# Optimization experiments

Hardware: AMD Instinct MI355X
Metric: run time of the kernel (lower is better)

## Reference

```python
import jax, jax.numpy as jnp
import numpy as np

B0, K, H, W = 8, 1, 512, 512
S, CS, NMS, M = 25, 51, 5, 2048
REG_W, COV_POW = 1.0, 0.5

def _gauss_kernel(n):
    x = jnp.linspace(-1.0, 1.0, n)
    g = jnp.exp(-x * x / 0.5)
    return g / g.sum()

def _conv1d2d(x, k1d, horizontal, pad_h, pad_w):
    # x: [B,1,H,W]; replicates torch F.conv2d with the given (possibly asymmetric) padding
    kern = k1d.reshape(1, 1, 1, -1) if horizontal else k1d.reshape(1, 1, -1, 1)
    return jax.lax.conv_general_dilated(x, kern, (1, 1), [(pad_h, pad_h), (pad_w, pad_w)],
                                        dimension_numbers=("NCHW", "OIHW", "NCHW"))

def bilinear_sample(img, pts):
    # img [B,C,H,W], pts [B,N,2] (x,y in [-1,1]); grid_sample bilinear, align_corners=False, zero padding
    Bb, C, Hh, Ww = img.shape
    x = (pts[..., 0] + 1.0) * 0.5 * Ww - 0.5
    y = (pts[..., 1] + 1.0) * 0.5 * Hh - 0.5
    x0 = jnp.floor(x); y0 = jnp.floor(y)
    wx = x - x0; wy = y - y0
    x0i = x0.astype(jnp.int32); y0i = y0.astype(jnp.int32)
    flat = img.reshape(Bb, C, Hh * Ww)
    def tap(yi, xi, w):
        ok = ((yi >= 0) & (yi < Hh) & (xi >= 0) & (xi < Ww)).astype(img.dtype)
        idx = jnp.clip(yi, 0, Hh - 1) * Ww + jnp.clip(xi, 0, Ww - 1)  # [B,N]
        v = jnp.take_along_axis(flat, idx[:, None, :], axis=2)        # [B,C,N]
        return v * (w * ok)[:, None, :]
    return (tap(y0i, x0i, (1 - wy) * (1 - wx)) + tap(y0i, x0i + 1, (1 - wy) * wx)
            + tap(y0i + 1, x0i, wy * (1 - wx)) + tap(y0i + 1, x0i + 1, wy * wx))

def compute_matchability(keypoint_p, has_depth, Bt):
    G = _gauss_kernel(S)
    # NOTE: faithful to original asymmetric padding bug: pad H while convolving along W, then pad W while convolving along H
    s = _conv1d2d(keypoint_p.reshape(Bt, 1, H, W), G, True, S // 2, 0)
    s = _conv1d2d(s, G, False, 0, S // 2)
    log_p_hat = jax.nn.log_softmax(jnp.log(s.reshape(Bt, H * W) + 1e-8), axis=-1)
    sd = _conv1d2d(has_depth.reshape(Bt, 1, H, W), G, True, 0, S // 2)
    sd = _conv1d2d(sd, G, False, S // 2, 0).reshape(Bt, H * W)
    p = sd / sd.sum(-1, keepdims=True)
    return jnp.sum(jnp.where(p > 0, p * (jnp.log(jnp.maximum(p, 1e-30)) - log_p_hat), 0.0), axis=-1)

def sample_keypoints(sm):
    # sm [B,H,W]; coverage-reweighted NMS + top-k (topk=True, subpixel=False)
    wcov = jnp.exp(-jnp.square(jnp.linspace(-2.0, 2.0, CS)))
    ld = _conv1d2d(((sm + 1e-6) * 1e4)[:, None], wcov, True, 0, CS // 2)
    ld = _conv1d2d(ld, wcov, False, CS // 2, 0)[:, 0]
    sm = sm * (ld + 1e-8) ** (-COV_POW)
    p = NMS // 2
    mx = jax.lax.reduce_window(sm, -jnp.inf, jax.lax.max, (1, NMS, NMS), (1, 1, 1),
                               [(0, 0), (p, p), (p, p)])
    sm = sm * (sm == mx)
    _, inds = jax.lax.top_k(sm.reshape(-1, H * W), M)
    xs = (jnp.arange(W) + 0.5) * 2.0 / W - 1.0
    ys = (jnp.arange(H) + 0.5) * 2.0 / H - 1.0
    grid = jnp.stack(jnp.meshgrid(xs, ys, indexing="xy"), axis=-1).reshape(H * W, 2)
    return jnp.take(grid, inds, axis=0)  # [B,M,2] normalized (x,y)

def masked_log_softmax(logits, mask):
    return jax.nn.log_softmax(jnp.where(mask, logits, -1e9), axis=-1)

def _reward(d):
    return jnp.exp(-100.0 * d)

def _forward(scoremap, gt_warp_A2B, gt_warp_B2A, valid_A2B, valid_B2A, has_depth):
    sg = jax.lax.stop_gradient
    lA = scoremap[:B0].reshape(B0, K, H * W)
    lB = scoremap[B0:].reshape(B0, K, H * W)
    logits = jnp.concatenate([lA, lB], 0)                                   # [2B,K,HW]
    kp_p = jax.nn.softmax(logits.reshape(2 * B0, K * H * W), -1).reshape(2 * B0, K, H * W).sum(1)
    match_loss = compute_matchability(kp_p, sg(has_depth), 2 * B0).mean()
    # sparse branch is under torch.set_grad_enabled(False)
    kpts_A = sample_keypoints(sg(kp_p[:B0]).reshape(B0, H, W))
    kpts_B = sample_keypoints(sg(kp_p[B0:]).reshape(B0, H, W))
    kpts_A2B = bilinear_sample(sg(gt_warp_A2B[..., 2:]).transpose(0, 3, 1, 2), kpts_A).transpose(0, 2, 1)
    kpts_B2A = bilinear_sample(sg(gt_warp_B2A[..., 2:]).transpose(0, 3, 1, 2), kpts_B).transpose(0, 2, 1)
    legit_A2B = bilinear_sample(sg(valid_A2B)[:, None], kpts_A)[:, 0] > 0   # [B,M]
    legit_B2A = bilinear_sample(sg(valid_B2A)[:, None], kpts_B)[:, 0] > 0
    dA = jnp.sqrt(jnp.sum(jnp.square(kpts_A2B[:, :, None] - kpts_B[:, None]), -1) + 1e-12).min(-1)
    dB = jnp.sqrt(jnp.sum(jnp.square(kpts_B2A[:, :, None] - kpts_A[:, None]), -1) + 1e-12).min(-1)
    rA = _reward(dA); rB = _reward(dB)
    slA = bilinear_sample(lA.reshape(B0, 1, H, W), kpts_A)[:, 0]            # [B,M]
    slB = bilinear_sample(lB.reshape(B0, 1, H, W), kpts_B)[:, 0]
    lpA = masked_log_softmax(slA, legit_A2B)
    lpB = masked_log_softmax(slB, legit_B2A)
    sparse = -jnp.sum(jnp.where(legit_A2B, rA * lpA, 0.0)) - jnp.sum(jnp.where(legit_B2A, rB * lpB, 0.0))
    return sparse + REG_W * match_loss

def setup_inputs() -> dict:
    key = jax.random.key(0)
    ks = jax.random.split(key, 6)
    scoremap = jax.random.normal(ks[0], (2 * B0, K, H, W), jnp.float32)
    gt_warp_A2B = jax.random.uniform(ks[1], (B0, H, W, 4), jnp.float32, -1.0, 1.0)
    gt_warp_B2A = jax.random.uniform(ks[2], (B0, H, W, 4), jnp.float32, -1.0, 1.0)
    valid_A2B = (jax.random.uniform(ks[3], (B0, H, W)) > 0.3).astype(jnp.float32)
    valid_B2A = (jax.random.uniform(ks[4], (B0, H, W)) > 0.3).astype(jnp.float32)
    has_depth = (jax.random.uniform(ks[5], (2 * B0, H, W)) > 0.3).astype(jnp.float32)
    return dict(scoremap=scoremap, gt_warp_A2B=gt_warp_A2B, gt_warp_B2A=gt_warp_B2A,
                valid_A2B=valid_A2B, valid_B2A=valid_B2A, has_depth=has_depth)

def reference(scoremap, gt_warp_A2B, gt_warp_B2A, valid_A2B, valid_B2A, has_depth):
    return _forward(scoremap, gt_warp_A2B, gt_warp_B2A, valid_A2B, valid_B2A, has_depth)
```

## Files before the change

### kernel.cpp

```cpp
#include <hip/hip_runtime.h>

#define HH 512
#define WW 512
#define HW_ 262144
#define NIMG 16
#define MK 2048
#define CAPB 4096
#define SCAP 32768
#define SBUFN 768

static constexpr size_t OFF_B1    = 16777216;
static constexpr size_t OFF_SMALL = 50331648;
static constexpr size_t OFF_SEL  = 4194304;
static constexpr size_t OFF_BND  = 4325376;
static constexpr size_t OFF_PP   = 4849664;
static constexpr size_t OFF_WXp  = 5111808;
static constexpr size_t OFF_WYp  = 5242880;
static constexpr size_t OFF_LG   = 5373952;
static constexpr size_t OFF_SL   = 5505024;
static constexpr size_t OFF_PMIN = 5636096;
static constexpr size_t OFF_HIST = 33554432;
static constexpr size_t OFF_SURV = 33554432 + 4194304;

#define CSTRIDE 32

__device__ __forceinline__ float wred64(float v) {
  for (int m = 1; m < 64; m <<= 1) v += __shfl_xor(v, m);
  return v;
}

__device__ __forceinline__ void g25_wave0(float* g) {
  int t = threadIdx.x;
  if (t < 64) {
    float raw = 0.0f;
    if (t < 25) {
      float x = -1.0f + (float)t * (2.0f / 24.0f);
      raw = expf(-(x * x) / 0.5f);
    }
    float s = raw;
    for (int m = 1; m < 64; m <<= 1) s += __shfl_xor(s, m);
    if (t < 25) g[t] = raw / s;
  }
}
__device__ __forceinline__ void w51_wave0(float* wc) {
  int t = threadIdx.x;
  if (t < 51) {
    float x = -2.0f + (float)t * (4.0f / 50.0f);
    wc[t] = expf(-x * x);
  }
}

template<int B>
__device__ __forceinline__ float brsum(float v, float* red) {
  int t = threadIdx.x;
  red[t] = v; __syncthreads();
  for (int s = B >> 1; s > 0; s >>= 1) {
    if (t < s) red[t] += red[t + s];
    __syncthreads();
  }
  float r = red[0]; __syncthreads();
  return r;
}
template<int B>
__device__ __forceinline__ float brmax(float v, float* red) {
  int t = threadIdx.x;
  red[t] = v; __syncthreads();
  for (int s = B >> 1; s > 0; s >>= 1) {
    if (t < s) red[t] = fmaxf(red[t], red[t + s]);
    __syncthreads();
  }
  float r = red[0]; __syncthreads();
  return r;
}

__global__ void __launch_bounds__(256)
k_pre(const float* __restrict__ x, const float* __restrict__ hd, float* A,
      float* sume, float* sumS, float* Zb) {
  __shared__ float g[25];
  __shared__ float gp[26];
  __shared__ float red[12];
  int tid = threadIdx.x;
  g25_wave0(g);
  if (tid == 0) {
    float c = 0.0f;
    gp[0] = 0.0f;
    for (int k = 0; k < 25; k++) { c += g[k]; gp[k + 1] = c; }
  }
  size_t base = (size_t)blockIdx.x * 1024;
  size_t e = base + tid * 4;
  float4 xs = *(const float4*)(x + e);
  float4 hs = *(const float4*)(hd + e);
  __syncthreads();
  int rem = (int)(e & (HW_ - 1));
  int y = rem >> 9, x0 = rem & 511;
  float wv;
  {
    int k0 = y - 499; if (k0 < 0) k0 = 0;
    int k1 = y + 12;  if (k1 > 24) k1 = 24;
    wv = gp[k1 + 1] - gp[k0];
  }
  float cwv[4], cpv[4];
#pragma unroll
  for (int q = 0; q < 4; q++) {
    int i = x0 + q;
    int lo = i - 487; if (lo < 0) lo = 0;
    int hi = i;       if (hi > 24) hi = 24;
    cwv[q] = gp[hi + 1] - gp[lo];
    int lo2 = i - 499; if (lo2 < 0) lo2 = 0;
    int hi2 = i + 12;  if (hi2 > 24) hi2 = 24;
    cpv[q] = gp[hi2 + 1] - gp[lo2];
  }
  float e0 = expf(xs.x), e1 = expf(xs.y), e2 = expf(xs.z), e3 = expf(xs.w);
  *(float4*)(A + e) = make_float4(e0, e1, e2, e3);
  float r0 = (e0 + e1) + (e2 + e3);
  float r1 = (e0 * cwv[0] + e1 * cwv[1] + e2 * cwv[2] + e3 * cwv[3]) * wv;
  float r2 = (hs.x * cpv[0] + hs.y * cpv[1] + hs.z * cpv[2] + hs.w * cpv[3]) * wv;
  r0 = wred64(r0); r1 = wred64(r1); r2 = wred64(r2);
  int wid = tid >> 6;
  if ((tid & 63) == 0) { red[wid] = r0; red[4 + wid] = r1; red[8 + wid] = r2; }
  __syncthreads();
  if (tid == 0) {
    int img = (int)(base >> 18);
    atomicAdd(&sume[img * CSTRIDE], red[0] + red[1] + red[2] + red[3]);
    atomicAdd(&sumS[img * CSTRIDE], red[4] + red[5] + red[6] + red[7]);
    atomicAdd(&Zb[img * CSTRIDE], red[8] + red[9] + red[10] + red[11]);
  }
}

__global__ void __launch_bounds__(256)
k_hconv(const float* __restrict__ A, const float* __restrict__ hd,
        const float* __restrict__ sume, float* b12) {
  __shared__ __align__(16) float ta[512];
  __shared__ __align__(16) float th[536];
  __shared__ float g[25];
  int tid = threadIdx.x;
  int blk = blockIdx.x;
  int img = blk >> 9;
  size_t rowoff = (size_t)blk * 512;
  g25_wave0(g);
  ((float2*)ta)[tid] = *(const float2*)(A + rowoff + tid * 2);
  ((float2*)(th + 12))[tid] = *(const float2*)(hd + rowoff + tid * 2);
  if (tid < 12) { th[tid] = 0.0f; th[524 + tid] = 0.0f; }
  __syncthreads();
  float inv = 1.0f / sume[img * CSTRIDE];
  int j = 2 * tid;
  float v1a = 0.0f, v1b = 0.0f;
  if (tid >= 6 && tid <= 249) {
    float w[26];
#pragma unroll
    for (int d = 0; d < 26; d++) w[d] = ta[j - 12 + d];
#pragma unroll
    for (int d = 0; d < 25; d++) {
      v1a = fmaf(g[d], w[d], v1a);
      v1b = fmaf(g[d], w[d + 1], v1b);
    }
  }
  float v2a = 0.0f, v2b = 0.0f;
  {
    float u[26];
#pragma unroll
    for (int d = 0; d < 26; d++) u[d] = th[j + d];
#pragma unroll
    for (int d = 0; d < 25; d++) {
      v2a = fmaf(g[d], u[d], v2a);
      v2b = fmaf(g[d], u[d + 1], v2b);
    }
  }
  *(float4*)(b12 + (rowoff + j) * 2) =
      make_float4(v1a * inv, v2a, v1b * inv, v2b);
}

__global__ void __launch_bounds__(256)
k_match(const float* __restrict__ b12,
        const float* __restrict__ sume, const float* sumS, const float* Zb,
        float* macc) {
  __shared__ float g[40];
  __shared__ float red4[4];
  int tid = threadIdx.x;
  g25_wave0(g);
  if (tid >= 25 && tid < 40) g[tid] = 0.0f;
  int blk = blockIdx.x;
  int img = blk >> 6;
  int ty = (blk >> 3) & 7;
  int tx = blk & 7;
  int y0 = ty * 64, x0 = tx * 64;
  const float* base12 = b12 + (size_t)img * HW_ * 2;
  float Z = Zb[img * CSTRIDE];
  float invs = 1.0f / sume[img * CSTRIDE];
  float logS = logf(sumS[img * CSTRIDE] * invs + (float)HW_ * 1e-8f);
  __syncthreads();
  int seg = tid >> 6;
  int c = tid & 63;
  int r0 = seg * 16;
  const float* colp = base12 + (size_t)(x0 + c) * 2;
  float s[16], d[16], wreg[16];
#pragma unroll
  for (int jj = 0; jj < 16; jj++) { s[jj] = 0.f; d[jj] = 0.f; wreg[jj] = 0.f; }
  int ybase = y0 + r0 - 12;
#pragma unroll
  for (int i = 0; i < 40; i++) {
    int y = ybase + i;
    float vx = 0.0f, vy = 0.0f;
    if ((unsigned)y < 512u) {
      float2 v = *(const float2*)(colp + (size_t)y * 1024);
      vx = v.x; vy = v.y;
    }
#pragma unroll
    for (int jj = 15; jj >= 1; jj--) wreg[jj] = wreg[jj - 1];
    wreg[0] = g[i];
#pragma unroll
    for (int jj = 0; jj < 16; jj++) {
      s[jj] = fmaf(wreg[jj], vx, s[jj]);
      d[jj] = fmaf(wreg[jj], vy, d[jj]);
    }
  }
  float acc = 0.0f;
#pragma unroll
  for (int jj = 0; jj < 16; jj++) {
    float p = d[jj] / Z;
    if (p > 0.0f)
      acc += p * (logf(fmaxf(p, 1e-30f)) - (logf(s[jj] + 1e-8f) - logS));
  }
  acc = wred64(acc);
  if ((tid & 63) == 0) red4[tid >> 6] = acc;
  __syncthreads();
  if (tid == 0)
    atomicAdd(macc, red4[0] + red4[1] + red4[2] + red4[3]);
}

__global__ void __launch_bounds__(256)
k_h51(const float* __restrict__ A, const float* __restrict__ sume, float* out,
      unsigned* __restrict__ hist) {
  __shared__ float wc[51];
  __shared__ __align__(16) float ta[564];
  int tid = threadIdx.x;
  int blk = blockIdx.x;
  int img = blk >> 9;
  size_t rowoff = (size_t)blk * 512;
  w51_wave0(wc);
  if (tid < 32)
    ((uint4*)hist)[(size_t)blk * 32 + tid] = make_uint4(0u, 0u, 0u, 0u);
  float s1 = 1e4f / sume[img * CSTRIDE];
  for (int i = tid; i < 562; i += 256) {
    int j = i - 25;
    ta[i] = ((unsigned)j < 512u) ? fmaf(A[rowoff + j], s1, 1e-2f) : 0.0f;
  }
  __syncthreads();
  int j = 2 * tid;
  float w[52];
#pragma unroll
  for (int d = 0; d < 52; d++) w[d] = ta[j + d];
  float va = 0.0f, vb = 0.0f;
#pragma unroll
  for (int d = 0; d < 51; d++) {
    va = fmaf(wc[d], w[d], va);
    vb = fmaf(wc[d], w[d + 1], vb);
  }
  ((float2*)out)[blk * 256 + tid] = make_float2(va, vb);
}

__global__ void __launch_bounds__(512, 6)
k_smwnms(const float* __restrict__ A, const float* __restrict__ sume,
         const float* __restrict__ b1,
         unsigned long long* surv, unsigned* scnt, unsigned* hist) {
  __shared__ float wc[53];
  __shared__ __align__(16) float tb1[119 * 68];
  __shared__ __align__(16) float tsm[68 * 68];
  __shared__ unsigned lcnt;
  __shared__ unsigned gbase;
  float* hm = tb1;
  unsigned long long* sbuf = (unsigned long long*)(tb1 + 4352);
  int tid = threadIdx.x;
  w51_wave0(wc);
  if (tid == 51 || tid == 52) wc[tid] = 0.0f;
  if (tid == 0) lcnt = 0;
  int blk = blockIdx.x;
  int img = blk >> 6;
  int ty = (blk >> 3) & 7;
  int tx = blk & 7;
  int y0 = ty * 64, x0 = tx * 64;
  const float* base = b1 + (size_t)img * HW_;
  {
    float2 vreg[8];
    int laddr[8];
#pragma unroll
    for (int k = 0; k < 8; k++) {
      int i = tid + k * 512;
      bool ok = (i < 119 * 34);
      int r = i / 34, c2 = i - r * 34;
      int y = y0 + r - 27;
      int x = x0 + c2 * 2 - 2;
      float2 v = make_float2(0.0f, 0.0f);
      if (ok && (unsigned)y < 512u && (unsigned)x < 512u)
        v = *(const float2*)(base + (size_t)y * 512 + x);
      vreg[k] = v;
      laddr[k] = ok ? (r * 68 + c2 * 2) : -1;
    }
#pragma unroll
    for (int k = 0; k < 8; k++)
      if (laddr[k] >= 0) *(float2*)(tb1 + laddr[k]) = vreg[k];
  }
  __syncthreads();
  float inv = 1.0f / sume[img * CSTRIDE];
  const float* abase = A + (size_t)img * HW_;
  if (tid < 23 * 17) {
    int rg = tid / 17, cg = tid - rg * 17;
    int r0 = rg * 3, c0 = cg * 4;
    int nr = (r0 <= 65) ? 3 : 2;
    float2 apre[3][2];
#pragma unroll
    for (int jj = 0; jj < 3; jj++) {
      int y = y0 + r0 + jj - 2;
      int xb = x0 + c0 - 2;
      apre[jj][0] = make_float2(0.f, 0.f);
      apre[jj][1] = make_float2(0.f, 0.f);
      if ((unsigned)y < 512u) {
        const float* ar = abase + (size_t)y * 512;
        if ((unsigned)xb < 512u) apre[jj][0] = *(const float2*)(ar + xb);
        if ((unsigned)(xb + 2) < 512u) apre[jj][1] = *(const float2*)(ar + xb + 2);
      }
    }
    float a0x = 0.f, a0y = 0.f, a0z = 0.f, a0w = 0.f;
    float a1x = 0.f, a1y = 0.f, a1z = 0.f, a1w = 0.f;
    float a2x = 0.f, a2y = 0.f, a2z = 0.f, a2w = 0.f;
    float w1 = 0.f, w2 = 0.f;
    const float* tp = tb1 + r0 * 68 + c0;
#pragma unroll 4
    for (int i = 0; i < 53; i++) {
      float4 v = *(const float4*)(tp + i * 68);
      float w0 = wc[i];
      a0x = fmaf(w0, v.x, a0x); a0y = fmaf(w0, v.y, a0y);
      a0z = fmaf(w0, v.z, a0z); a0w = fmaf(w0, v.w, a0w);
      a1x = fmaf(w1, v.x, a1x); a1y = fmaf(w1, v.y, a1y);
      a1z = fmaf(w1, v.z, a1z); a1w = fmaf(w1, v.w, a1w);
      a2x = fmaf(w2, v.x, a2x); a2y = fmaf(w2, v.y, a2y);
      a2z = fmaf(w2, v.z, a2z); a2w = fmaf(w2, v.w, a2w);
      w2 = w1; w1 = w0;
    }
    auto storerow = [&](int jj, float ax, float ay, float az, float aw,
                        float2 p0, float2 p1) {
      int r = r0 + jj;
      int y = y0 + r - 2;
      int xb = x0 + c0 - 2;
      float4 res = make_float4(-3.4e38f, -3.4e38f, -3.4e38f, -3.4e38f);
      if ((unsigned)y < 512u) {
        if ((unsigned)xb < 512u) {
          res.x = (p0.x * inv) / sqrtf(ax + 1e-8f);
          res.y = (p0.y * inv) / sqrtf(ay + 1e-8f);
        }
        if ((unsigned)(xb + 2) < 512u) {
          res.z = (p1.x * inv) / sqrtf(az + 1e-8f);
          res.w = (p1.y * inv) / sqrtf(aw + 1e-8f);
        }
      }
      *(float4*)(tsm + r * 68 + c0) = res;
    };
    storerow(0, a0x, a0y, a0z, a0w, apre[0][0], apre[0][1]);
    storerow(1, a1x, a1y, a1z, a1w, apre[1][0], apre[1][1]);
    if (nr == 3) storerow(2, a2x, a2y, a2z, a2w, apre[2][0], apre[2][1]);
  }
  __syncthreads();
  for (int i = tid; i < 68 * 16; i += 512) {
    int r = i >> 4, cg = i & 15;
    const float* row = tsm + r * 68 + cg * 4;
    float4 v0 = *(const float4*)(row);
    float4 v1 = *(const float4*)(row + 4);
    float p01 = fmaxf(v0.x, v0.y), p12 = fmaxf(v0.y, v0.z);
    float p23 = fmaxf(v0.z, v0.w), p34 = fmaxf(v0.w, v1.x);
    float p45 = fmaxf(v1.x, v1.y), p56 = fmaxf(v1.y, v1.z);
    float m0 = fmaxf(fmaxf(p01, p23), v1.x);
    float m1 = fmaxf(fmaxf(p12, p34), v1.y);
    float m2 = fmaxf(fmaxf(p23, p45), v1.z);
    float m3 = fmaxf(fmaxf(p34, p56), v1.w);
    *(float4*)(hm + r * 64 + cg * 4) = make_float4(m0, m1, m2, m3);
  }
  __syncthreads();
  for (int k0 = 0; k0 < 2; k0++) {
    int i = tid + k0 * 512;
    int r = i >> 4, cb = (i & 15) * 4;
    const float* tp2 = tsm + (r + 2) * 68 + cb + 2;
    float2 va = *(const float2*)(tp2);
    float2 vb = *(const float2*)(tp2 + 2);
    float4 m0 = *(const float4*)(hm + r * 64 + cb);
    float4 m1 = *(const float4*)(hm + (r + 1) * 64 + cb);
    float4 m2 = *(const float4*)(hm + (r + 2) * 64 + cb);
    float4 m3 = *(const float4*)(hm + (r + 3) * 64 + cb);
    float4 m4 = *(const float4*)(hm + (r + 4) * 64 + cb);
    float Mx = fmaxf(fmaxf(m0.x, m1.x), fmaxf(fmaxf(m2.x, m3.x), m4.x));
    float My = fmaxf(fmaxf(m0.y, m1.y), fmaxf(fmaxf(m2.y, m3.y), m4.y));
    float Mz = fmaxf(fmaxf(m0.z, m1.z), fmaxf(fmaxf(m2.z, m3.z), m4.z));
    float Mw = fmaxf(fmaxf(m0.w, m1.w), fmaxf(fmaxf(m2.w, m3.w), m4.w));
    auto keepf = [&](float vk, float Mk, int k) {
      if (vk == Mk && vk != 0.0f) {
        unsigned p = atomicAdd(&lcnt, 1u);
        unsigned bits = __float_as_uint(vk);
        unsigned idx = (unsigned)((y0 + r) * 512 + x0 + cb + k);
        if (p < SBUFN)
          sbuf[p] = ((unsigned long long)bits << 32) |
                    (unsigned long long)(idx ^ 0xFFFFFFFFu);
        atomicAdd(&hist[(size_t)img * 65536 + (bits >> 16)], 1u);
      }
    };
    keepf(va.x, Mx, 0); keepf(va.y, My, 1);
    keepf(vb.x, Mz, 2); keepf(vb.y, Mw, 3);
  }
  __syncthreads();
  unsigned total = lcnt; if (total > SBUFN) total = SBUFN;
  if (tid == 0) gbase = atomicAdd(&scnt[img * CSTRIDE], total);
  __syncthreads();
  unsigned gb = gbase;
  for (unsigned i = tid; i < total; i += 512) {
    unsigned p = gb + i;
    if (p < SCAP) surv[(size_t)img * SCAP + p] = sbuf[i];
  }
}

__global__ void __launch_bounds__(1024)
k_thresh(const unsigned* __restrict__ hist, unsigned* Tb, unsigned* needb) {
  int img = blockIdx.x;
  const unsigned* h = hist + (size_t)img * 65536;
  __shared__ unsigned wsum[16];
  __shared__ unsigned wpre[16];
  int t = threadIdx.x;
  int b0 = 65472 - 64 * t;
  const uint4* hv = (const uint4*)(h + b0);
  unsigned s = 0;
#pragma unroll
  for (int k = 0; k < 16; k++) {
    uint4 u = hv[k];
    s += u.x + u.y + u.z + u.w;
  }
  if (b0 == 0) s += 0x00100000u - h[0];
  unsigned inc = s;
  for (int m = 1; m < 64; m <<= 1) {
    unsigned o = __shfl_up(inc, m);
    if ((t & 63) >= m) inc += o;
  }
  if ((t & 63) == 63) wsum[t >> 6] = inc;
  __syncthreads();
  if (t < 16) {
    unsigned p = 0;
    for (int k = 0; k < 16; k++) if (k < t) p += wsum[k];
    wpre[t] = p;
  }
  __syncthreads();
  unsigned pre = wpre[t >> 6] + inc - s;
  if (pre < MK && pre + s >= MK) {
    unsigned c = pre;
    for (int k = 0; k < 64; k++) {
      int bin = 65535 - (t * 64 + k);
      unsigned cnt = (bin == 0) ? 0x00100000u : h[bin];
      if (c + cnt >= MK) { Tb[img * CSTRIDE] = (unsigned)bin; needb[img * CSTRIDE] = MK - c; break; }
      c += cnt;
    }
  }
}

__global__ void k_collect(const unsigned long long* __restrict__ surv,
                          const unsigned* __restrict__ scnt,
                          const unsigned* __restrict__ Tb,
                          unsigned* selcnt, unsigned* sel,
                          unsigned* bcnt, unsigned long long* bnd) {
  int blk = blockIdx.x;
  int img = blk >> 7;
  int i = (blk & 127) * 256 + threadIdx.x;
  unsigned cnt = scnt[img * CSTRIDE]; if (cnt > SCAP) cnt = SCAP;
  unsigned long long entry = ((unsigned)i < cnt) ? surv[(size_t)img * SCAP + i] : 0ull;
  unsigned bits = (unsigned)(entry >> 32);
  unsigned bin = bits >> 16;
  unsigned T = Tb[img * CSTRIDE];
  bool ok = (unsigned)i < cnt;
  bool c1 = ok && (bin > T);
  bool c2 = ok && (bin == T);
  int lane = threadIdx.x & 63;
  unsigned long long lowmask = (1ull << lane) - 1ull;

  unsigned long long m1 = __ballot(c1);
  if (m1) {
    int leader = __ffsll(m1) - 1;
    unsigned base = 0;
    if (lane == leader) base = atomicAdd(&selcnt[img * CSTRIDE], (unsigned)__popcll(m1));
    base = __shfl(base, leader);
    if (c1) {
      unsigned p = base + (unsigned)__popcll(m1 & lowmask);
      if (p < MK) sel[img * MK + p] = (unsigned)(entry & 0xFFFFFFFFull) ^ 0xFFFFFFFFu;
    }
  }
  unsigned long long m2 = __ballot(c2);
  if (m2) {
    int leader = __ffsll(m2) - 1;
    unsigned base = 0;
    if (lane == leader) base = atomicAdd(&bcnt[img * CSTRIDE], (unsigned)__popcll(m2));
    base = __shfl(base, leader);
    if (c2) {
      unsigned p = base + (unsigned)__popcll(m2 & lowmask);
      if (p < CAPB) bnd[(size_t)img * CAPB + p] = entry;
    }
  }
}

__global__ void __launch_bounds__(1024)
k_finsel(const unsigned long long* __restrict__ bnd, const unsigned* bcnt,
         const unsigned* needb, const unsigned* selcnt, unsigned* sel) {
  int img = blockIdx.x;
  __shared__ unsigned long long key[CAPB];
  unsigned bn = bcnt[img * CSTRIDE];
  int n = (bn < CAPB) ? (int)bn : CAPB;
  int np2 = 2;
  while (np2 < n) np2 <<= 1;
  int t = threadIdx.x;
  for (int k = t; k < np2; k += 1024)
    key[k] = (k < n) ? bnd[(size_t)img * CAPB + k] : 0ull;
  __syncthreads();
  for (int sz = 2; sz <= np2; sz <<= 1) {
    for (int st = sz >> 1; st > 0; st >>= 1) {
      for (int i = t; i < np2; i += 1024) {
        int l = i ^ st;
        if (l > i) {
          unsigned long long a = key[i], b = key[l];
          bool up = ((i & sz) == 0);
          if (up ? (a < b) : (a > b)) { key[i] = b; key[l] = a; }
        }
      }
      __syncthreads();
    }
  }
  unsigned c1 = selcnt[img * CSTRIDE]; if (c1 > MK) c1 = MK;
  unsigned need = needb[img * CSTRIDE];
  unsigned kk = need; if (kk > MK - c1) kk = MK - c1;
  for (unsigned m = t; m < MK - c1; m += 1024) {
    unsigned v = 0u;
    if (m < kk && m < (unsigned)n)
      v = (unsigned)(key[m] & 0xFFFFFFFFull) ^ 0xFFFFFFFFu;
    sel[img * MK + c1 + m] = v;
  }
}

__global__ void k_prep(const unsigned* __restrict__ sel, const float* __restrict__ scoremap,
                       const float* __restrict__ gtA, const float* __restrict__ gtB,
                       const float* __restrict__ vA, const float* __restrict__ vB,
                       float2* pp, float* wx, float* wy, float* lg, float* sl) {
  int t = blockIdx.x * 256 + threadIdx.x;
  int img = t >> 11;
  unsigned idx = sel[t] & (HW_ - 1);
  int h = idx >> 9, w = idx & 511;
  pp[t] = make_float2((w + 0.5f) * (2.0f / 512.0f) - 1.0f,
                      (h + 0.5f) * (2.0f / 512.0f) - 1.0f);
  int b = (img < 8) ? img : img - 8;
  const float* gt = (img < 8) ? gtA : gtB;
  const float* vv = (img < 8) ? vA : vB;
  size_t pix = (size_t)b * HW_ + idx;
  float2 gxy = *(const float2*)(gt + pix * 4 + 2);
  wx[t] = gxy.x;
  wy[t] = gxy.y;
  lg[t] = (vv[pix] > 0.0f) ? 1.0f : 0.0f;
  sl[t] = scoremap[(size_t)img * HW_ + idx];
}

__global__ void __launch_bounds__(256)
k_mindist(const float2* __restrict__ pp,
          const float* __restrict__ wx, const float* __restrict__ wy,
          float* pmin) {
  __shared__ float2 opp[512];
  int blk = blockIdx.x;
  int img = blk >> 5;
  int qc = (blk >> 2) & 7;
  int oc = blk & 3;
  const float2* ob = pp + (size_t)(img ^ 8) * MK + oc * 512;
  for (int k = threadIdx.x; k < 512; k += 256) opp[k] = ob[k];
  __syncthreads();
  int m = img * MK + qc * 256 + threadIdx.x;
  float ax = wx[m], ay = wy[m];
  float d[8];
#pragma unroll
  for (int u = 0; u < 8; u++) d[u] = 3.4e38f;
  for (int n = 0; n < 512; n += 8) {
#pragma unroll
    for (int u = 0; u < 8; u++) {
      float2 o = opp[n + u];
      float dx = ax - o.x, dy = ay - o.y;
      d[u] = fminf(d[u], fmaf(dx, dx, dy * dy));
    }
  }
  float d2 = fminf(fminf(fminf(d[0], d[1]), fminf(d[2], d[3])),
                   fminf(fminf(d[4], d[5]), fminf(d[6], d[7])));
  pmin[oc * (NIMG * MK) + m] = d2;
}

__global__ void __launch_bounds__(1024)
k_loss(const float* __restrict__ sl, const float* __restrict__ lg,
       const float* __restrict__ pmin, float* sacc, float* macc, float* out,
       unsigned* ldone) {
  int img = blockIdx.x;
  __shared__ float red[1024];
  int t = threadIdx.x;
  int i0 = img * MK + t, i1 = i0 + 1024;
  float s0 = sl[i0], s1 = sl[i1];
  float g0 = lg[i0], g1 = lg[i1];
  float l0 = (g0 > 0.0f) ? s0 : -1e9f;
  float l1 = (g1 > 0.0f) ? s1 : -1e9f;
  float mx = brmax<1024>(fmaxf(l0, l1), red);
  float se = brsum<1024>(expf(l0 - mx) + expf(l1 - mx), red);
  float lse = mx + logf(se);
  const int ST = NIMG * MK;
  float a = 0.0f;
  if (g0 > 0.0f) {
    float mn = fminf(fminf(pmin[i0], pmin[ST + i0]),
                     fminf(pmin[2 * ST + i0], pmin[3 * ST + i0]));
    float r0 = expf(-100.0f * sqrtf(mn + 1e-12f));
    a += r0 * (s0 - lse);
  }
  if (g1 > 0.0f) {
    float mn = fminf(fminf(pmin[i1], pmin[ST + i1]),
                     fminf(pmin[2 * ST + i1], pmin[3 * ST + i1]));
    float r1 = expf(-100.0f * sqrtf(mn + 1e-12f));
    a += r1 * (s1 - lse);
  }
  float tot = brsum<1024>(a, red);
  if (t == 0) {
    atomicAdd(sacc, -tot);
    __threadfence();
    unsigned dnum = atomicAdd(ldone, 1u);
    if (dnum == NIMG - 1) {
      float sv = atomicAdd(sacc, 0.0f);
      float mv = atomicAdd(macc, 0.0f);
      out[0] = sv + mv * (1.0f / 16.0f);
    }
  }
}

extern "C" void kernel_launch(void* const* d_in, const int* in_sizes, int n_in,
                              void* d_out, int out_size, void* d_ws, size_t ws_size,
                              hipStream_t stream) {
  const float* scoremap = (const float*)d_in[0];
  const float* gtA = (const float*)d_in[1];
  const float* gtB = (const float*)d_in[2];
  const float* vA  = (const float*)d_in[3];
  const float* vB  = (const float*)d_in[4];
  const float* hd  = (const float*)d_in[5];

  char* ws = (char*)d_ws;
  float* A   = (float*)(ws);
  float* B12 = (float*)(ws + OFF_B1);
  float* B1p = (float*)(ws + OFF_B1);

  char* sm = ws + OFF_SMALL;
  float*    sume   = (float*)(sm + 0);
  float*    sumS   = (float*)(sm + 2048);
  float*    Zb     = (float*)(sm + 4096);
  unsigned* Tb     = (unsigned*)(sm + 6144);
  unsigned* needb  = (unsigned*)(sm + 8192);
  unsigned* selcnt = (unsigned*)(sm + 10240);
  unsigned* bcnt   = (unsigned*)(sm + 12288);
  float*    macc   = (float*)(sm + 14336);
  float*    sacc   = (float*)(sm + 14464);
  unsigned* scnt   = (unsigned*)(sm + 16384);
  unsigned* ldone  = (unsigned*)(sm + 20480);

  unsigned* hist = (unsigned*)(ws + OFF_HIST);
  unsigned long long* surv = (unsigned long long*)(ws + OFF_SURV);
  unsigned* sel  = (unsigned*)(ws + OFF_SEL);
  unsigned long long* bnd = (unsigned long long*)(ws + OFF_BND);
  float2* pp = (float2*)(ws + OFF_PP);
  float* wx = (float*)(ws + OFF_WXp);
  float* wy = (float*)(ws + OFF_WYp);
  float* lg = (float*)(ws + OFF_LG);
  float* sl = (float*)(ws + OFF_SL);
  float* pmin = (float*)(ws + OFF_PMIN);

  float* out = (float*)d_out;

  hipMemsetAsync(sm, 0, 32768, stream);

  k_pre<<<4096, 256, 0, stream>>>(scoremap, hd, A, sume, sumS, Zb);

  k_hconv<<<8192, 256, 0, stream>>>(A, hd, sume, B12);
  k_match<<<1024, 256, 0, stream>>>(B12, sume, sumS, Zb, macc);

  k_h51<<<8192, 256, 0, stream>>>(A, sume, B1p, hist);

  k_smwnms<<<1024, 512, 0, stream>>>(A, sume, B1p, surv, scnt, hist);
  k_thresh<<<16, 1024, 0, stream>>>(hist, Tb, needb);
  k_collect<<<2048, 256, 0, stream>>>(surv, scnt, Tb, selcnt, sel, bcnt, bnd);
  k_finsel<<<16, 1024, 0, stream>>>(bnd, bcnt, needb, selcnt, sel);

  k_prep<<<128, 256, 0, stream>>>(sel, scoremap, gtA, gtB, vA, vB, pp, wx, wy, lg, sl);
  k_mindist<<<512, 256, 0, stream>>>(pp, wx, wy, pmin);
  k_loss<<<16, 1024, 0, stream>>>(sl, lg, pmin, sacc, macc, out, ldone);
}
```

Measured before the change: 287.0 us.

## Fuse threshold/collect/finsel/prep into one select kernel and fold loss into mindist

Merges the four post-NMS selection kernels (threshold scan, collect, boundary sort, keypoint prep) into a single per-image block that compacts survivors with shared-memory atomics and sorts boundary entries in LDS. It also folds the loss reduction into k_mindist: the last block to finish for each image, detected through an atomic counter, does the softmax and loss using coherent loads. This removes four launches and the global round trips for sel/bnd, at the cost of less parallelism in the collect step, which now uses 16 blocks instead of 2048.

```diff
diff --git a/kernel.cpp b/kernel.cpp
--- a/kernel.cpp
+++ b/kernel.cpp
@@ -11,8 +11,6 @@
 
 static constexpr size_t OFF_B1    = 16777216;
 static constexpr size_t OFF_SMALL = 50331648;
-static constexpr size_t OFF_SEL  = 4194304;
-static constexpr size_t OFF_BND  = 4325376;
 static constexpr size_t OFF_PP   = 4849664;
 static constexpr size_t OFF_WXp  = 5111808;
 static constexpr size_t OFF_WYp  = 5242880;
@@ -29,6 +27,10 @@
   return v;
 }
 
+__device__ __forceinline__ float coh_loadf(const float* p) {
+  return __hip_atomic_load(p, __ATOMIC_RELAXED, __HIP_MEMORY_SCOPE_AGENT);
+}
+
 __device__ __forceinline__ void g25_wave0(float* g) {
   int t = threadIdx.x;
   if (t < 64) {
@@ -48,29 +50,6 @@
     float x = -2.0f + (float)t * (4.0f / 50.0f);
     wc[t] = expf(-x * x);
   }
-}
-
-template<int B>
-__device__ __forceinline__ float brsum(float v, float* red) {
-  int t = threadIdx.x;
-  red[t] = v; __syncthreads();
-  for (int s = B >> 1; s > 0; s >>= 1) {
-    if (t < s) red[t] += red[t + s];
-    __syncthreads();
-  }
-  float r = red[0]; __syncthreads();
-  return r;
-}
-template<int B>
-__device__ __forceinline__ float brmax(float v, float* red) {
-  int t = threadIdx.x;
-  red[t] = v; __syncthreads();
-  for (int s = B >> 1; s > 0; s >>= 1) {
-    if (t < s) red[t] = fmaxf(red[t], red[t + s]);
-    __syncthreads();
-  }
-  float r = red[0]; __syncthreads();
-  return r;
 }
 
 __global__ void __launch_bounds__(256)
@@ -416,12 +395,23 @@
 }
 
 __global__ void __launch_bounds__(1024)
-k_thresh(const unsigned* __restrict__ hist, unsigned* Tb, unsigned* needb) {
+k_select(const unsigned long long* __restrict__ surv,
+         const unsigned* __restrict__ scnt,
+         const unsigned* __restrict__ hist,
+         const float* __restrict__ scoremap,
+         const float* __restrict__ gtA, const float* __restrict__ gtB,
+         const float* __restrict__ vA, const float* __restrict__ vB,
+         float2* pp, float* wx, float* wy, float* lg, float* sl) {
   int img = blockIdx.x;
-  const unsigned* h = hist + (size_t)img * 65536;
+  __shared__ unsigned long long key[CAPB];
+  __shared__ unsigned selbuf[MK];
   __shared__ unsigned wsum[16];
   __shared__ unsigned wpre[16];
+  __shared__ unsigned cnts[2];
+  __shared__ unsigned TbS, needS;
   int t = threadIdx.x;
+  if (t < 2) cnts[t] = 0;
+  const unsigned* h = hist + (size_t)img * 65536;
   int b0 = 65472 - 64 * t;
   const uint4* hv = (const uint4*)(h + b0);
   unsigned s = 0;
@@ -450,67 +440,35 @@
     for (int k = 0; k < 64; k++) {
       int bin = 65535 - (t * 64 + k);
       unsigned cnt = (bin == 0) ? 0x00100000u : h[bin];
-      if (c + cnt >= MK) { Tb[img * CSTRIDE] = (unsigned)bin; needb[img * CSTRIDE] = MK - c; break; }
+      if (c + cnt >= MK) { TbS = (unsigned)bin; needS = MK - c; break; }
       c += cnt;
     }
   }
-}
-
-__global__ void k_collect(const unsigned long long* __restrict__ surv,
-                          const unsigned* __restrict__ scnt,
-                          const unsigned* __restrict__ Tb,
-                          unsigned* selcnt, unsigned* sel,
-                          unsigned* bcnt, unsigned long long* bnd) {
-  int blk = blockIdx.x;
-  int img = blk >> 7;
-  int i = (blk & 127) * 256 + threadIdx.x;
+  __syncthreads();
+  unsigned T = TbS, need = needS;
   unsigned cnt = scnt[img * CSTRIDE]; if (cnt > SCAP) cnt = SCAP;
-  unsigned long long entry = ((unsigned)i < cnt) ? surv[(size_t)img * SCAP + i] : 0ull;
-  unsigned bits = (unsigned)(entry >> 32);
-  unsigned bin = bits >> 16;
-  unsigned T = Tb[img * CSTRIDE];
-  bool ok = (unsigned)i < cnt;
-  bool c1 = ok && (bin > T);
-  bool c2 = ok && (bin == T);
-  int lane = threadIdx.x & 63;
-  unsigned long long lowmask = (1ull << lane) - 1ull;
-
-  unsigned long long m1 = __ballot(c1);
-  if (m1) {
-    int leader = __ffsll(m1) - 1;
-    unsigned base = 0;
-    if (lane == leader) base = atomicAdd(&selcnt[img * CSTRIDE], (unsigned)__popcll(m1));
-    base = __shfl(base, leader);
-    if (c1) {
-      unsigned p = base + (unsigned)__popcll(m1 & lowmask);
-      if (p < MK) sel[img * MK + p] = (unsigned)(entry & 0xFFFFFFFFull) ^ 0xFFFFFFFFu;
-    }
-  }
-  unsigned long long m2 = __ballot(c2);
-  if (m2) {
-    int leader = __ffsll(m2) - 1;
-    unsigned base = 0;
-    if (lane == leader) base = atomicAdd(&bcnt[img * CSTRIDE], (unsigned)__popcll(m2));
-    base = __shfl(base, leader);
-    if (c2) {
-      unsigned p = base + (unsigned)__popcll(m2 & lowmask);
-      if (p < CAPB) bnd[(size_t)img * CAPB + p] = entry;
-    }
-  }
-}
-
-__global__ void __launch_bounds__(1024)
-k_finsel(const unsigned long long* __restrict__ bnd, const unsigned* bcnt,
-         const unsigned* needb, const unsigned* selcnt, unsigned* sel) {
-  int img = blockIdx.x;
-  __shared__ unsigned long long key[CAPB];
-  unsigned bn = bcnt[img * CSTRIDE];
+  const unsigned long long* sv = surv + (size_t)img * SCAP;
+  for (unsigned i = t; i < SCAP; i += 1024) {
+    if (i < cnt) {
+      unsigned long long entry = sv[i];
+      unsigned bin = (unsigned)(entry >> 48);
+      if (bin > T) {
+        unsigned p = atomicAdd(&cnts[0], 1u);
+        if (p < MK) selbuf[p] = (unsigned)(entry & 0xFFFFFFFFull) ^ 0xFFFFFFFFu;
+      } else if (bin == T) {
+        unsigned p = atomicAdd(&cnts[1], 1u);
+        if (p < CAPB) key[p] = entry;
+      }
+    }
+  }
+  __syncthreads();
+  unsigned c1 = cnts[0]; if (c1 > MK) c1 = MK;
+  unsigned bn = cnts[1];
   int n = (bn < CAPB) ? (int)bn : CAPB;
   int np2 = 2;
   while (np2 < n) np2 <<= 1;
-  int t = threadIdx.x;
   for (int k = t; k < np2; k += 1024)
-    key[k] = (k < n) ? bnd[(size_t)img * CAPB + k] : 0ull;
+    if (k >= n) key[k] = 0ull;
   __syncthreads();
   for (int sz = 2; sz <= np2; sz <<= 1) {
     for (int st = sz >> 1; st > 0; st >>= 1) {
@@ -525,43 +483,42 @@
       __syncthreads();
     }
   }
-  unsigned c1 = selcnt[img * CSTRIDE]; if (c1 > MK) c1 = MK;
-  unsigned need = needb[img * CSTRIDE];
   unsigned kk = need; if (kk > MK - c1) kk = MK - c1;
   for (unsigned m = t; m < MK - c1; m += 1024) {
     unsigned v = 0u;
     if (m < kk && m < (unsigned)n)
       v = (unsigned)(key[m] & 0xFFFFFFFFull) ^ 0xFFFFFFFFu;
-    sel[img * MK + c1 + m] = v;
-  }
-}
-
-__global__ void k_prep(const unsigned* __restrict__ sel, const float* __restrict__ scoremap,
-                       const float* __restrict__ gtA, const float* __restrict__ gtB,
-                       const float* __restrict__ vA, const float* __restrict__ vB,
-                       float2* pp, float* wx, float* wy, float* lg, float* sl) {
-  int t = blockIdx.x * 256 + threadIdx.x;
-  int img = t >> 11;
-  unsigned idx = sel[t] & (HW_ - 1);
-  int h = idx >> 9, w = idx & 511;
-  pp[t] = make_float2((w + 0.5f) * (2.0f / 512.0f) - 1.0f,
-                      (h + 0.5f) * (2.0f / 512.0f) - 1.0f);
+    selbuf[c1 + m] = v;
+  }
+  __syncthreads();
   int b = (img < 8) ? img : img - 8;
   const float* gt = (img < 8) ? gtA : gtB;
   const float* vv = (img < 8) ? vA : vB;
-  size_t pix = (size_t)b * HW_ + idx;
-  float2 gxy = *(const float2*)(gt + pix * 4 + 2);
-  wx[t] = gxy.x;
-  wy[t] = gxy.y;
-  lg[t] = (vv[pix] > 0.0f) ? 1.0f : 0.0f;
-  sl[t] = scoremap[(size_t)img * HW_ + idx];
+  for (int q = t; q < MK; q += 1024) {
+    int tt = img * MK + q;
+    unsigned idx = selbuf[q] & (HW_ - 1);
+    int hh = idx >> 9, wp = idx & 511;
+    pp[tt] = make_float2((wp + 0.5f) * (2.0f / 512.0f) - 1.0f,
+                         (hh + 0.5f) * (2.0f / 512.0f) - 1.0f);
+    size_t pix = (size_t)b * HW_ + idx;
+    float2 gxy = *(const float2*)(gt + pix * 4 + 2);
+    wx[tt] = gxy.x;
+    wy[tt] = gxy.y;
+    lg[tt] = (vv[pix] > 0.0f) ? 1.0f : 0.0f;
+    sl[tt] = scoremap[(size_t)img * HW_ + idx];
+  }
 }
 
 __global__ void __launch_bounds__(256)
 k_mindist(const float2* __restrict__ pp,
           const float* __restrict__ wx, const float* __restrict__ wy,
-          float* pmin) {
+          float* pmin,
+          const float* __restrict__ sl, const float* __restrict__ lg,
+          float* sacc, float* macc, float* out,
+          unsigned* mdone, unsigned* ldone) {
   __shared__ float2 opp[512];
+  __shared__ unsigned rank_s;
+  __shared__ float red[1024];
   int blk = blockIdx.x;
   int img = blk >> 5;
   int qc = (blk >> 2) & 7;
@@ -585,38 +542,73 @@
   float d2 = fminf(fminf(fminf(d[0], d[1]), fminf(d[2], d[3])),
                    fminf(fminf(d[4], d[5]), fminf(d[6], d[7])));
   pmin[oc * (NIMG * MK) + m] = d2;
-}
-
-__global__ void __launch_bounds__(1024)
-k_loss(const float* __restrict__ sl, const float* __restrict__ lg,
-       const float* __restrict__ pmin, float* sacc, float* macc, float* out,
-       unsigned* ldone) {
-  int img = blockIdx.x;
-  __shared__ float red[1024];
+  __syncthreads();
+  if (threadIdx.x == 0) {
+    __threadfence();
+    rank_s = atomicAdd(&mdone[img * CSTRIDE], 1u);
+  }
+  __syncthreads();
+  if (rank_s != 31) return;
+  __threadfence();
   int t = threadIdx.x;
-  int i0 = img * MK + t, i1 = i0 + 1024;
-  float s0 = sl[i0], s1 = sl[i1];
-  float g0 = lg[i0], g1 = lg[i1];
-  float l0 = (g0 > 0.0f) ? s0 : -1e9f;
-  float l1 = (g1 > 0.0f) ? s1 : -1e9f;
-  float mx = brmax<1024>(fmaxf(l0, l1), red);
-  float se = brsum<1024>(expf(l0 - mx) + expf(l1 - mx), red);
-  float lse = mx + logf(se);
   const int ST = NIMG * MK;
-  float a = 0.0f;
-  if (g0 > 0.0f) {
-    float mn = fminf(fminf(pmin[i0], pmin[ST + i0]),
-                     fminf(pmin[2 * ST + i0], pmin[3 * ST + i0]));
-    float r0 = expf(-100.0f * sqrtf(mn + 1e-12f));
-    a += r0 * (s0 - lse);
-  }
-  if (g1 > 0.0f) {
-    float mn = fminf(fminf(pmin[i1], pmin[ST + i1]),
-                     fminf(pmin[2 * ST + i1], pmin[3 * ST + i1]));
-    float r1 = expf(-100.0f * sqrtf(mn + 1e-12f));
-    a += r1 * (s1 - lse);
-  }
-  float tot = brsum<1024>(a, red);
+  float l0s[4], l1s[4], s0s[4], s1s[4], g0s[4], g1s[4];
+#pragma unroll
+  for (int u = 0; u < 4; u++) {
+    int t0 = t + u * 256;
+    int i0 = img * MK + t0, i1 = i0 + 1024;
+    float s0 = sl[i0], s1 = sl[i1];
+    float g0 = lg[i0], g1 = lg[i1];
+    s0s[u] = s0; s1s[u] = s1; g0s[u] = g0; g1s[u] = g1;
+    float l0 = (g0 > 0.0f) ? s0 : -1e9f;
+    float l1 = (g1 > 0.0f) ? s1 : -1e9f;
+    l0s[u] = l0; l1s[u] = l1;
+    red[t0] = fmaxf(l0, l1);
+  }
+  __syncthreads();
+  for (int sd = 512; sd > 0; sd >>= 1) {
+    for (int k = t; k < sd; k += 256) red[k] = fmaxf(red[k], red[k + sd]);
+    __syncthreads();
+  }
+  float mx = red[0];
+  __syncthreads();
+#pragma unroll
+  for (int u = 0; u < 4; u++) {
+    int t0 = t + u * 256;
+    red[t0] = expf(l0s[u] - mx) + expf(l1s[u] - mx);
+  }
+  __syncthreads();
+  for (int sd = 512; sd > 0; sd >>= 1) {
+    for (int k = t; k < sd; k += 256) red[k] += red[k + sd];
+    __syncthreads();
+  }
+  float lse = mx + logf(red[0]);
+  __syncthreads();
+#pragma unroll
+  for (int u = 0; u < 4; u++) {
+    int t0 = t + u * 256;
+    int i0 = img * MK + t0, i1 = i0 + 1024;
+    float a = 0.0f;
+    if (g0s[u] > 0.0f) {
+      float mn = fminf(fminf(coh_loadf(&pmin[i0]), coh_loadf(&pmin[ST + i0])),
+                       fminf(coh_loadf(&pmin[2 * ST + i0]), coh_loadf(&pmin[3 * ST + i0])));
+      float r0 = expf(-100.0f * sqrtf(mn + 1e-12f));
+      a += r0 * (s0s[u] - lse);
+    }
+    if (g1s[u] > 0.0f) {
+      float mn = fminf(fminf(coh_loadf(&pmin[i1]), coh_loadf(&pmin[ST + i1])),
+                       fminf(coh_loadf(&pmin[2 * ST + i1]), coh_loadf(&pmin[3 * ST + i1])));
+      float r1 = expf(-100.0f * sqrtf(mn + 1e-12f));
+      a += r1 * (s1s[u] - lse);
+    }
+    red[t0] = a;
+  }
+  __syncthreads();
+  for (int sd = 512; sd > 0; sd >>= 1) {
+    for (int k = t; k < sd; k += 256) red[k] += red[k + sd];
+    __syncthreads();
+  }
+  float tot = red[0];
   if (t == 0) {
     atomicAdd(sacc, -tot);
     __threadfence();
@@ -648,19 +640,14 @@
   float*    sume   = (float*)(sm + 0);
   float*    sumS   = (float*)(sm + 2048);
   float*    Zb     = (float*)(sm + 4096);
-  unsigned* Tb     = (unsigned*)(sm + 6144);
-  unsigned* needb  = (unsigned*)(sm + 8192);
-  unsigned* selcnt = (unsigned*)(sm + 10240);
-  unsigned* bcnt   = (unsigned*)(sm + 12288);
   float*    macc   = (float*)(sm + 14336);
   float*    sacc   = (float*)(sm + 14464);
   unsigned* scnt   = (unsigned*)(sm + 16384);
   unsigned* ldone  = (unsigned*)(sm + 20480);
+  unsigned* mdone  = (unsigned*)(sm + 24576);
 
   unsigned* hist = (unsigned*)(ws + OFF_HIST);
   unsigned long long* surv = (unsigned long long*)(ws + OFF_SURV);
-  unsigned* sel  = (unsigned*)(ws + OFF_SEL);
-  unsigned long long* bnd = (unsigned long long*)(ws + OFF_BND);
   float2* pp = (float2*)(ws + OFF_PP);
   float* wx = (float*)(ws + OFF_WXp);
   float* wy = (float*)(ws + OFF_WYp);
@@ -680,11 +667,10 @@
   k_h51<<<8192, 256, 0, stream>>>(A, sume, B1p, hist);
 
   k_smwnms<<<1024, 512, 0, stream>>>(A, sume, B1p, surv, scnt, hist);
-  k_thresh<<<16, 1024, 0, stream>>>(hist, Tb, needb);
-  k_collect<<<2048, 256, 0, stream>>>(surv, scnt, Tb, selcnt, sel, bcnt, bnd);
-  k_finsel<<<16, 1024, 0, stream>>>(bnd, bcnt, needb, selcnt, sel);
-
-  k_prep<<<128, 256, 0, stream>>>(sel, scoremap, gtA, gtB, vA, vB, pp, wx, wy, lg, sl);
-  k_mindist<<<512, 256, 0, stream>>>(pp, wx, wy, pmin);
-  k_loss<<<16, 1024, 0, stream>>>(sl, lg, pmin, sacc, macc, out, ldone);
-}
+
+  k_select<<<16, 1024, 0, stream>>>(surv, scnt, hist, scoremap, gtA, gtB,
+                                    vA, vB, pp, wx, wy, lg, sl);
+
+  k_mindist<<<512, 256, 0, stream>>>(pp, wx, wy, pmin, sl, lg,
+                                     sacc, macc, out, mdone, ldone);
+}
```

Result: slower. 307.1 us (+7.0%).

## Halve smoothing/NMS tile width and fuse final selection with keypoint prep

Applied to the files above, without the earlier changes.

The smoothed-score NMS kernel now uses 64x32 tiles with 256-thread blocks (2048 blocks) instead of 64x64 tiles with 512 threads, shrinking shared memory per block so more blocks can be resident. Narrower tiles re-read a relatively larger halo, since the 27-row vertical halo stays the same while column reuse drops. Separately, the final boundary-sort selection kernel is fused with the keypoint prep kernel, which removes one launch and the round trip of the tail selection indices through global memory. The prep work now runs on only 16 blocks instead of 128, so its gathers are less parallel.

```diff
diff --git a/kernel.cpp b/kernel.cpp
--- a/kernel.cpp
+++ b/kernel.cpp
@@ -259,52 +259,52 @@
   ((float2*)out)[blk * 256 + tid] = make_float2(va, vb);
 }
 
-__global__ void __launch_bounds__(512, 6)
+__global__ void __launch_bounds__(256, 5)
 k_smwnms(const float* __restrict__ A, const float* __restrict__ sume,
          const float* __restrict__ b1,
          unsigned long long* surv, unsigned* scnt, unsigned* hist) {
   __shared__ float wc[53];
-  __shared__ __align__(16) float tb1[119 * 68];
-  __shared__ __align__(16) float tsm[68 * 68];
+  __shared__ __align__(16) float tb1[119 * 36];
+  __shared__ __align__(16) float tsm[68 * 36];
   __shared__ unsigned lcnt;
   __shared__ unsigned gbase;
   float* hm = tb1;
-  unsigned long long* sbuf = (unsigned long long*)(tb1 + 4352);
+  unsigned long long* sbuf = (unsigned long long*)(tb1 + 2176);
   int tid = threadIdx.x;
   w51_wave0(wc);
   if (tid == 51 || tid == 52) wc[tid] = 0.0f;
   if (tid == 0) lcnt = 0;
   int blk = blockIdx.x;
-  int img = blk >> 6;
-  int ty = (blk >> 3) & 7;
-  int tx = blk & 7;
-  int y0 = ty * 64, x0 = tx * 64;
+  int img = blk >> 7;
+  int ty = (blk >> 4) & 7;
+  int tx = blk & 15;
+  int y0 = ty * 64, x0 = tx * 32;
   const float* base = b1 + (size_t)img * HW_;
   {
-    float2 vreg[8];
-    int laddr[8];
-#pragma unroll
-    for (int k = 0; k < 8; k++) {
-      int i = tid + k * 512;
-      bool ok = (i < 119 * 34);
-      int r = i / 34, c2 = i - r * 34;
+    float2 vreg[9];
+    int laddr[9];
+#pragma unroll
+    for (int k = 0; k < 9; k++) {
+      int i = tid + k * 256;
+      bool ok = (i < 119 * 18);
+      int r = i / 18, c2 = i - r * 18;
       int y = y0 + r - 27;
       int x = x0 + c2 * 2 - 2;
       float2 v = make_float2(0.0f, 0.0f);
       if (ok && (unsigned)y < 512u && (unsigned)x < 512u)
         v = *(const float2*)(base + (size_t)y * 512 + x);
       vreg[k] = v;
-      laddr[k] = ok ? (r * 68 + c2 * 2) : -1;
-    }
-#pragma unroll
-    for (int k = 0; k < 8; k++)
+      laddr[k] = ok ? (r * 36 + c2 * 2) : -1;
+    }
+#pragma unroll
+    for (int k = 0; k < 9; k++)
       if (laddr[k] >= 0) *(float2*)(tb1 + laddr[k]) = vreg[k];
   }
   __syncthreads();
   float inv = 1.0f / sume[img * CSTRIDE];
   const float* abase = A + (size_t)img * HW_;
-  if (tid < 23 * 17) {
-    int rg = tid / 17, cg = tid - rg * 17;
+  if (tid < 23 * 9) {
+    int rg = tid / 9, cg = tid - rg * 9;
     int r0 = rg * 3, c0 = cg * 4;
     int nr = (r0 <= 65) ? 3 : 2;
     float2 apre[3][2];
@@ -324,10 +324,10 @@
     float a1x = 0.f, a1y = 0.f, a1z = 0.f, a1w = 0.f;
     float a2x = 0.f, a2y = 0.f, a2z = 0.f, a2w = 0.f;
     float w1 = 0.f, w2 = 0.f;
-    const float* tp = tb1 + r0 * 68 + c0;
+    const float* tp = tb1 + r0 * 36 + c0;
 #pragma unroll 4
     for (int i = 0; i < 53; i++) {
-      float4 v = *(const float4*)(tp + i * 68);
+      float4 v = *(const float4*)(tp + i * 36);
       float w0 = wc[i];
       a0x = fmaf(w0, v.x, a0x); a0y = fmaf(w0, v.y, a0y);
       a0z = fmaf(w0, v.z, a0z); a0w = fmaf(w0, v.w, a0w);
@@ -353,16 +353,16 @@
           res.w = (p1.y * inv) / sqrtf(aw + 1e-8f);
         }
       }
-      *(float4*)(tsm + r * 68 + c0) = res;
+      *(float4*)(tsm + r * 36 + c0) = res;
     };
     storerow(0, a0x, a0y, a0z, a0w, apre[0][0], apre[0][1]);
     storerow(1, a1x, a1y, a1z, a1w, apre[1][0], apre[1][1]);
     if (nr == 3) storerow(2, a2x, a2y, a2z, a2w, apre[2][0], apre[2][1]);
   }
   __syncthreads();
-  for (int i = tid; i < 68 * 16; i += 512) {
-    int r = i >> 4, cg = i & 15;
-    const float* row = tsm + r * 68 + cg * 4;
+  for (int i = tid; i < 68 * 8; i += 256) {
+    int r = i >> 3, cg = i & 7;
+    const float* row = tsm + r * 36 + cg * 4;
     float4 v0 = *(const float4*)(row);
     float4 v1 = *(const float4*)(row + 4);
     float p01 = fmaxf(v0.x, v0.y), p12 = fmaxf(v0.y, v0.z);
@@ -372,20 +372,20 @@
     float m1 = fmaxf(fmaxf(p12, p34), v1.y);
     float m2 = fmaxf(fmaxf(p23, p45), v1.z);
     float m3 = fmaxf(fmaxf(p34, p56), v1.w);
-    *(float4*)(hm + r * 64 + cg * 4) = make_float4(m0, m1, m2, m3);
+    *(float4*)(hm + r * 32 + cg * 4) = make_float4(m0, m1, m2, m3);
   }
   __syncthreads();
   for (int k0 = 0; k0 < 2; k0++) {
-    int i = tid + k0 * 512;
-    int r = i >> 4, cb = (i & 15) * 4;
-    const float* tp2 = tsm + (r + 2) * 68 + cb + 2;
+    int i = tid + k0 * 256;
+    int r = i >> 3, cb = (i & 7) * 4;
+    const float* tp2 = tsm + (r + 2) * 36 + cb + 2;
     float2 va = *(const float2*)(tp2);
     float2 vb = *(const float2*)(tp2 + 2);
-    float4 m0 = *(const float4*)(hm + r * 64 + cb);
-    float4 m1 = *(const float4*)(hm + (r + 1) * 64 + cb);
-    float4 m2 = *(const float4*)(hm + (r + 2) * 64 + cb);
-    float4 m3 = *(const float4*)(hm + (r + 3) * 64 + cb);
-    float4 m4 = *(const float4*)(hm + (r + 4) * 64 + cb);
+    float4 m0 = *(const float4*)(hm + r * 32 + cb);
+    float4 m1 = *(const float4*)(hm + (r + 1) * 32 + cb);
+    float4 m2 = *(const float4*)(hm + (r + 2) * 32 + cb);
+    float4 m3 = *(const float4*)(hm + (r + 3) * 32 + cb);
+    float4 m4 = *(const float4*)(hm + (r + 4) * 32 + cb);
     float Mx = fmaxf(fmaxf(m0.x, m1.x), fmaxf(fmaxf(m2.x, m3.x), m4.x));
     float My = fmaxf(fmaxf(m0.y, m1.y), fmaxf(fmaxf(m2.y, m3.y), m4.y));
     float Mz = fmaxf(fmaxf(m0.z, m1.z), fmaxf(fmaxf(m2.z, m3.z), m4.z));
@@ -409,7 +409,7 @@
   if (tid == 0) gbase = atomicAdd(&scnt[img * CSTRIDE], total);
   __syncthreads();
   unsigned gb = gbase;
-  for (unsigned i = tid; i < total; i += 512) {
+  for (unsigned i = tid; i < total; i += 256) {
     unsigned p = gb + i;
     if (p < SCAP) surv[(size_t)img * SCAP + p] = sbuf[i];
   }
@@ -500,8 +500,13 @@
 }
 
 __global__ void __launch_bounds__(1024)
-k_finsel(const unsigned long long* __restrict__ bnd, const unsigned* bcnt,
-         const unsigned* needb, const unsigned* selcnt, unsigned* sel) {
+k_fsp(const unsigned long long* __restrict__ bnd, const unsigned* bcnt,
+      const unsigned* needb, const unsigned* selcnt,
+      const unsigned* __restrict__ sel,
+      const float* __restrict__ scoremap,
+      const float* __restrict__ gtA, const float* __restrict__ gtB,
+      const float* __restrict__ vA, const float* __restrict__ vB,
+      float2* pp, float* wx, float* wy, float* lg, float* sl) {
   int img = blockIdx.x;
   __shared__ unsigned long long key[CAPB];
   unsigned bn = bcnt[img * CSTRIDE];
@@ -528,33 +533,31 @@
   unsigned c1 = selcnt[img * CSTRIDE]; if (c1 > MK) c1 = MK;
   unsigned need = needb[img * CSTRIDE];
   unsigned kk = need; if (kk > MK - c1) kk = MK - c1;
-  for (unsigned m = t; m < MK - c1; m += 1024) {
-    unsigned v = 0u;
-    if (m < kk && m < (unsigned)n)
-      v = (unsigned)(key[m] & 0xFFFFFFFFull) ^ 0xFFFFFFFFu;
-    sel[img * MK + c1 + m] = v;
-  }
-}
-
-__global__ void k_prep(const unsigned* __restrict__ sel, const float* __restrict__ scoremap,
-                       const float* __restrict__ gtA, const float* __restrict__ gtB,
-                       const float* __restrict__ vA, const float* __restrict__ vB,
-                       float2* pp, float* wx, float* wy, float* lg, float* sl) {
-  int t = blockIdx.x * 256 + threadIdx.x;
-  int img = t >> 11;
-  unsigned idx = sel[t] & (HW_ - 1);
-  int h = idx >> 9, w = idx & 511;
-  pp[t] = make_float2((w + 0.5f) * (2.0f / 512.0f) - 1.0f,
-                      (h + 0.5f) * (2.0f / 512.0f) - 1.0f);
   int b = (img < 8) ? img : img - 8;
   const float* gt = (img < 8) ? gtA : gtB;
   const float* vv = (img < 8) ? vA : vB;
-  size_t pix = (size_t)b * HW_ + idx;
-  float2 gxy = *(const float2*)(gt + pix * 4 + 2);
-  wx[t] = gxy.x;
-  wy[t] = gxy.y;
-  lg[t] = (vv[pix] > 0.0f) ? 1.0f : 0.0f;
-  sl[t] = scoremap[(size_t)img * HW_ + idx];
+  for (int q = t; q < MK; q += 1024) {
+    unsigned v;
+    if ((unsigned)q < c1) {
+      v = sel[img * MK + q];
+    } else {
+      unsigned m = (unsigned)q - c1;
+      v = 0u;
+      if (m < kk && m < (unsigned)n)
+        v = (unsigned)(key[m] & 0xFFFFFFFFull) ^ 0xFFFFFFFFu;
+    }
+    int tt = img * MK + q;
+    unsigned idx = v & (HW_ - 1);
+    int hh = idx >> 9, wp = idx & 511;
+    pp[tt] = make_float2((wp + 0.5f) * (2.0f / 512.0f) - 1.0f,
+                         (hh + 0.5f) * (2.0f / 512.0f) - 1.0f);
+    size_t pix = (size_t)b * HW_ + idx;
+    float2 gxy = *(const float2*)(gt + pix * 4 + 2);
+    wx[tt] = gxy.x;
+    wy[tt] = gxy.y;
+    lg[tt] = (vv[pix] > 0.0f) ? 1.0f : 0.0f;
+    sl[tt] = scoremap[(size_t)img * HW_ + idx];
+  }
 }
 
 __global__ void __launch_bounds__(256)
@@ -679,12 +682,13 @@
 
   k_h51<<<8192, 256, 0, stream>>>(A, sume, B1p, hist);
 
-  k_smwnms<<<1024, 512, 0, stream>>>(A, sume, B1p, surv, scnt, hist);
+  k_smwnms<<<2048, 256, 0, stream>>>(A, sume, B1p, surv, scnt, hist);
   k_thresh<<<16, 1024, 0, stream>>>(hist, Tb, needb);
   k_collect<<<2048, 256, 0, stream>>>(surv, scnt, Tb, selcnt, sel, bcnt, bnd);
-  k_finsel<<<16, 1024, 0, stream>>>(bnd, bcnt, needb, selcnt, sel);
-
-  k_prep<<<128, 256, 0, stream>>>(sel, scoremap, gtA, gtB, vA, vB, pp, wx, wy, lg, sl);
+
+  k_fsp<<<16, 1024, 0, stream>>>(bnd, bcnt, needb, selcnt, sel, scoremap,
+                                 gtA, gtB, vA, vB, pp, wx, wy, lg, sl);
+
   k_mindist<<<512, 256, 0, stream>>>(pp, wx, wy, pmin);
   k_loss<<<16, 1024, 0, stream>>>(sl, lg, pmin, sacc, macc, out, ldone);
 }
```

New measurement: 300.2 us. 4.6% more time.
